# Optimization experiments

Hardware: AMD Instinct MI355X
Metric: run time of the kernel (lower is better)

## Reference

```python
import jax, jax.numpy as jnp
import numpy as np

# Module hyperparameters (see init_kwargs)
P1, P2 = 32, 32      # num_patches_h, num_patches_w (256/8)
H1, W2 = 8, 8        # patch_size
CH = 3               # input channels
CI, SI = 768, 4      # num_cores, rfs_per_capsule (capsule_size=256, rf_size=64)
KOUT, LOUT = 256, 4  # output_cores, slots per output core
PROBA = 0.1          # connection_proba


def setup_inputs() -> dict:
    key = jax.random.key(0)
    kx, kc = jax.random.split(key)
    x = jax.random.normal(kx, (128, 256, 256, 3), dtype=jnp.float32)
    # fast_scrramble: fixed random-sparse binary connectivity tensor
    # [source_core, source_slot, dest_core, dest_slot]
    C = jax.random.bernoulli(kc, PROBA, (CI, SI, KOUT, LOUT)).astype(jnp.float32)
    return {"x": x, "C": C}


def reference(x, C):
    b = x.shape[0]
    # 'b (p1 h1) (p2 w2) c -> b p1 p2 h1 w2 c'
    x = x.reshape(b, P1, H1, P2, W2, CH).transpose(0, 1, 3, 2, 4, 5)
    # 'b p1 p2 h1 w2 c -> b h1 w2 (p1 p2 c)'
    x = x.transpose(0, 3, 4, 1, 2, 5).reshape(b, H1, W2, P1 * P2 * CH)
    # 'b h1 w2 (ci si) -> b ci si h1 w2'
    x = x.reshape(b, H1, W2, CI, SI).transpose(0, 3, 4, 1, 2)
    # Literal einsum from the source: no shared labels between operands,
    # so this is sum_{c,s} x (per b,h,w) times sum_{i,j} C (per k,l).
    return jnp.einsum('bcshw,ijkl->bklhw', x, C)
```

## Files before the change

kernel.cpp:

```cpp
#include <hip/hip_runtime.h>


__global__ __launch_bounds__(256) void reduce_C_kernel(const float* __restrict__ C,
                                                       float* __restrict__ sC) {
    const int col  = blockIdx.x * 256 + threadIdx.x;
    const int row0 = blockIdx.y * 32;
    const float* p = C + (size_t)row0 * 1024 + col;
    float s = 0.f;
#pragma unroll
    for (int r = 0; r < 32; ++r) s += p[r * 1024];
    atomicAdd(sC + col, s);
}

__global__ __launch_bounds__(192) void reduce_x_kernel(const float* __restrict__ x,
                                                       float* __restrict__ sx) {
    const int b  = blockIdx.y;
    const int y0 = blockIdx.x * 32;
    const int t  = threadIdx.x;
    const float* base = x + ((size_t)b * 256 + y0) * 768;

    float acc[8];
#pragma unroll
    for (int h = 0; h < 8; ++h) acc[h] = 0.f;

#pragma unroll
    for (int h = 0; h < 8; ++h) {
#pragma unroll
        for (int j = 0; j < 4; ++j) {
            const float* rowp = base + (size_t)(h + 8 * j) * 768;
#pragma unroll
            for (int it = 0; it < 4; ++it)
                acc[h] += rowp[it * 192 + t];
        }
    }

    __shared__ float lds[192][8];
#pragma unroll
    for (int h = 0; h < 8; ++h) lds[t][h] = acc[h];
    __syncthreads();

    if (t < 64) {
        const int h = t >> 3, w = t & 7;
        float s = 0.f;
#pragma unroll
        for (int g = 0; g < 8; ++g)
#pragma unroll
            for (int c = 0; c < 3; ++c)
                s += lds[g * 24 + w * 3 + c][h];
        atomicAdd(sx + b * 64 + t, s);
    }
}

__global__ __launch_bounds__(256) void expand_kernel(const float* __restrict__ sx,
                                                     const float* __restrict__ sC,
                                                     float4* __restrict__ out) {
    const int b   = blockIdx.y;
    const int idx = blockIdx.x * 256 + threadIdx.x;
    const int hw4 = idx & 15;
    const int kl  = idx >> 4;
    const float4 v = ((const float4*)(sx + b * 64))[hw4];
    const float  s = sC[kl];
    float4 r;
    r.x = v.x * s; r.y = v.y * s; r.z = v.z * s; r.w = v.w * s;
    out[(size_t)b * 16384 + idx] = r;
}

extern "C" void kernel_launch(void* const* d_in, const int* in_sizes, int n_in,
                              void* d_out, int out_size, void* d_ws, size_t ws_size,
                              hipStream_t stream) {
    const float* x = (const float*)d_in[0];
    const float* C = (const float*)d_in[1];
    float* out = (float*)d_out;

    float* sC = (float*)d_ws;
    float* sx = (float*)d_ws + 1024;

    hipMemsetAsync(d_ws, 0, (1024 + 8192) * sizeof(float), stream);

    reduce_C_kernel<<<dim3(4, 96),  256, 0, stream>>>(C, sC);
    reduce_x_kernel<<<dim3(8, 128), 192, 0, stream>>>(x, sx);
    expand_kernel<<<dim3(64, 128),  256, 0, stream>>>(sx, sC, (float4*)out);
}
```

Measured before the change: 171.4 us.

## Merge C and x reductions into one kernel with partials, drop memset and atomics

Combines the C reduction and the x reduction into a single launch, with the first 16 blocks reducing C and the rest reducing x using float4 loads. Each block writes its partial sums to workspace instead of using atomics, so the memset is gone. A finalize kernel sums the partials in LDS and writes the expanded output, with each block producing 2048 float4s. The intent is fewer launches, wider loads and no atomics, at the cost of extra LDS traffic and a second-level reduction.

```diff
diff --git a/kernel.cpp b/kernel.cpp
--- a/kernel.cpp
+++ b/kernel.cpp
@@ -1,83 +1,136 @@
 #include <hip/hip_runtime.h>
 
 
-__global__ __launch_bounds__(256) void reduce_C_kernel(const float* __restrict__ C,
-                                                       float* __restrict__ sC) {
-    const int col  = blockIdx.x * 256 + threadIdx.x;
-    const int row0 = blockIdx.y * 32;
-    const float* p = C + (size_t)row0 * 1024 + col;
-    float s = 0.f;
+__global__ __launch_bounds__(192) void reduce_partials(
+    const float4* __restrict__ x4,
+    const float4* __restrict__ C4,
+    float*  __restrict__ cpart,
+    float*  __restrict__ xpart)
+{
+    const int t   = threadIdx.x;
+    const int blk = blockIdx.x;
+
+    if (blk < 16) {
+        const size_t r0 = (size_t)blk * 192;
+        for (int c4 = t; c4 < 256; c4 += 192) {
+            const float4* p = C4 + r0 * 256 + c4;
+            float ax = 0, ay = 0, az = 0, aw = 0;
+            float bx = 0, by = 0, bz = 0, bw = 0;
+#pragma unroll 4
+            for (int r = 0; r < 192; r += 2) {
+                float4 v0 = p[0];
+                float4 v1 = p[256];
+                ax += v0.x; ay += v0.y; az += v0.z; aw += v0.w;
+                bx += v1.x; by += v1.y; bz += v1.z; bw += v1.w;
+                p += 512;
+            }
+            float4 s;
+            s.x = ax + bx; s.y = ay + by; s.z = az + bz; s.w = aw + bw;
+            ((float4*)cpart)[blk * 256 + c4] = s;
+        }
+        return;
+    }
+
+    const int xb    = blk - 16;
+    const int b     = xb >> 3;
+    const int chunk = xb & 7;
+    const float4* base = x4 + ((size_t)b * 256 + (size_t)chunk * 32) * 192 + t;
+
+    float4 acc[8];
 #pragma unroll
-    for (int r = 0; r < 32; ++r) s += p[r * 1024];
-    atomicAdd(sC + col, s);
-}
-
-__global__ __launch_bounds__(192) void reduce_x_kernel(const float* __restrict__ x,
-                                                       float* __restrict__ sx) {
-    const int b  = blockIdx.y;
-    const int y0 = blockIdx.x * 32;
-    const int t  = threadIdx.x;
-    const float* base = x + ((size_t)b * 256 + y0) * 768;
-
-    float acc[8];
-#pragma unroll
-    for (int h = 0; h < 8; ++h) acc[h] = 0.f;
+    for (int h = 0; h < 8; ++h) { acc[h].x = acc[h].y = acc[h].z = acc[h].w = 0.f; }
 
 #pragma unroll
     for (int h = 0; h < 8; ++h) {
 #pragma unroll
         for (int j = 0; j < 4; ++j) {
-            const float* rowp = base + (size_t)(h + 8 * j) * 768;
-#pragma unroll
-            for (int it = 0; it < 4; ++it)
-                acc[h] += rowp[it * 192 + t];
+            float4 v = base[(size_t)(h + 8 * j) * 192];
+            acc[h].x += v.x; acc[h].y += v.y; acc[h].z += v.z; acc[h].w += v.w;
         }
     }
 
-    __shared__ float lds[192][8];
+    __shared__ float4 ldsv[192][9];
+    __shared__ float  plane[8][193];
 #pragma unroll
-    for (int h = 0; h < 8; ++h) lds[t][h] = acc[h];
+    for (int h = 0; h < 8; ++h) ldsv[t][h] = acc[h];
+    __syncthreads();
+
+    {
+        const int h2  = t / 48;
+        const int tau = t - h2 * 48;
+#pragma unroll
+        for (int k = 0; k < 2; ++k) {
+            const int hh = h2 + 4 * k;
+            float4 s0 = ldsv[tau      ][hh];
+            float4 s1 = ldsv[tau +  48][hh];
+            float4 s2 = ldsv[tau +  96][hh];
+            float4 s3 = ldsv[tau + 144][hh];
+            plane[hh][4 * tau + 0] = s0.x + s1.x + s2.x + s3.x;
+            plane[hh][4 * tau + 1] = s0.y + s1.y + s2.y + s3.y;
+            plane[hh][4 * tau + 2] = s0.z + s1.z + s2.z + s3.z;
+            plane[hh][4 * tau + 3] = s0.w + s1.w + s2.w + s3.w;
+        }
+    }
     __syncthreads();
 
     if (t < 64) {
         const int h = t >> 3, w = t & 7;
         float s = 0.f;
 #pragma unroll
-        for (int g = 0; g < 8; ++g)
-#pragma unroll
-            for (int c = 0; c < 3; ++c)
-                s += lds[g * 24 + w * 3 + c][h];
-        atomicAdd(sx + b * 64 + t, s);
+        for (int g = 0; g < 8; ++g) {
+            const float* pp = &plane[h][24 * g + 3 * w];
+            s += pp[0] + pp[1] + pp[2];
+        }
+        xpart[xb * 64 + t] = s;
     }
 }
 
-__global__ __launch_bounds__(256) void expand_kernel(const float* __restrict__ sx,
-                                                     const float* __restrict__ sC,
-                                                     float4* __restrict__ out) {
+__global__ __launch_bounds__(256) void finalize_expand(
+    const float* __restrict__ xpart,
+    const float* __restrict__ cpart,
+    float4* __restrict__ out4)
+{
+    const int t   = threadIdx.x;
+    const int klc = blockIdx.x;
     const int b   = blockIdx.y;
-    const int idx = blockIdx.x * 256 + threadIdx.x;
-    const int hw4 = idx & 15;
-    const int kl  = idx >> 4;
-    const float4 v = ((const float4*)(sx + b * 64))[hw4];
-    const float  s = sC[kl];
-    float4 r;
-    r.x = v.x * s; r.y = v.y * s; r.z = v.z * s; r.w = v.w * s;
-    out[(size_t)b * 16384 + idx] = r;
+
+    __shared__ float4 sxv[16];
+    __shared__ float  scl[128];
+
+    if (t < 64) {
+        float s = 0.f;
+#pragma unroll
+        for (int j = 0; j < 8; ++j) s += xpart[((b << 3) + j) * 64 + t];
+        ((float*)sxv)[t] = s;
+    } else if (t < 192) {
+        const int c = klc * 128 + (t - 64);
+        float s = 0.f;
+#pragma unroll
+        for (int g = 0; g < 16; ++g) s += cpart[g * 1024 + c];
+        scl[t - 64] = s;
+    }
+    __syncthreads();
+
+    float4* ob = out4 + (size_t)b * 16384 + (size_t)klc * 2048;
+#pragma unroll
+    for (int k = 0; k < 8; ++k) {
+        const int idx = k * 256 + t;
+        const float4 v = sxv[idx & 15];
+        const float  s = scl[idx >> 4];
+        float4 r;
+        r.x = v.x * s; r.y = v.y * s; r.z = v.z * s; r.w = v.w * s;
+        ob[idx] = r;
+    }
 }
 
 extern "C" void kernel_launch(void* const* d_in, const int* in_sizes, int n_in,
                               void* d_out, int out_size, void* d_ws, size_t ws_size,
                               hipStream_t stream) {
-    const float* x = (const float*)d_in[0];
-    const float* C = (const float*)d_in[1];
-    float* out = (float*)d_out;
+    const float4* x4 = (const float4*)d_in[0];
+    const float4* C4 = (const float4*)d_in[1];
+    float* cpart = (float*)d_ws;
+    float* xpart = (float*)d_ws + 16384;
 
-    float* sC = (float*)d_ws;
-    float* sx = (float*)d_ws + 1024;
-
-    hipMemsetAsync(d_ws, 0, (1024 + 8192) * sizeof(float), stream);
-
-    reduce_C_kernel<<<dim3(4, 96),  256, 0, stream>>>(C, sC);
-    reduce_x_kernel<<<dim3(8, 128), 192, 0, stream>>>(x, sx);
-    expand_kernel<<<dim3(64, 128),  256, 0, stream>>>(sx, sC, (float4*)out);
+    reduce_partials<<<dim3(16 + 1024), 192, 0, stream>>>(x4, C4, cpart, xpart);
+    finalize_expand<<<dim3(8, 128),    256, 0, stream>>>(xpart, cpart, (float4*)d_out);
 }
```

Measured after the change: 189.9 us. +10.8%, slower.
